# Kernel optimization log

Hardware: AMD Instinct MI355X
Metric: run time of the kernel (lower is better)

## Reference

```python
import jax, jax.numpy as jnp
import numpy as np
import math

B, S, D = 4, 1024, 1024
H, DH = 16, 64
DFF = 4 * D
NEG = -1e9


def _layernorm(x, g, b, eps=1e-5):
    mu = jnp.mean(x, axis=-1, keepdims=True)
    var = jnp.var(x, axis=-1, keepdims=True)
    return (x - mu) * jax.lax.rsqrt(var + eps) * g + b


def setup_inputs() -> dict:
    key = jax.random.key(0)
    ks = jax.random.split(key, 12)
    inp = {
        "input": jax.random.normal(ks[0], (B, S, D), dtype=jnp.float32),
        # additive causal mask: 0 on/below diagonal, -1e9 above
        "causal_mask": jnp.where(
            jnp.tril(jnp.ones((S, S), dtype=bool)), 0.0, NEG
        ).astype(jnp.float32)[None, None],
        # additive padding mask: last 64 tokens of each sequence are padding
        "padding_mask": jnp.where(jnp.arange(S) < S - 64, 0.0, NEG)
        .astype(jnp.float32)[None, None, None, :]
        .repeat(B, axis=0),
        "ln1_g": jnp.ones((D,), jnp.float32), "ln1_b": jnp.zeros((D,), jnp.float32),
        "ln2_g": jnp.ones((D,), jnp.float32), "ln2_b": jnp.zeros((D,), jnp.float32),
        "ln3_g": jnp.ones((D,), jnp.float32), "ln3_b": jnp.zeros((D,), jnp.float32),
        "Wq": jax.random.normal(ks[1], (D, H * DH), jnp.float32) * 0.02,
        "bq": jnp.zeros((H * DH,), jnp.float32),
        "Wk": jax.random.normal(ks[2], (D, H * DH), jnp.float32) * 0.02,
        "bk": jnp.zeros((H * DH,), jnp.float32),
        "Wv": jax.random.normal(ks[3], (D, H * DH), jnp.float32) * 0.02,
        "bv": jnp.zeros((H * DH,), jnp.float32),
        "Wo": jax.random.normal(ks[4], (H * DH, D), jnp.float32) * 0.02,
        "bo": jnp.zeros((D,), jnp.float32),
        "W1": jax.random.normal(ks[5], (D, DFF), jnp.float32) * 0.02,
        "b1": jnp.zeros((DFF,), jnp.float32),
        "W2": jax.random.normal(ks[6], (DFF, D), jnp.float32) * 0.02,
        "b2": jnp.zeros((D,), jnp.float32),
    }
    return inp


def reference(input, causal_mask, padding_mask,
              ln1_g, ln1_b, ln2_g, ln2_b, ln3_g, ln3_b,
              Wq, bq, Wk, bk, Wv, bv, Wo, bo, W1, b1, W2, b2):
    x = _layernorm(input, ln1_g, ln1_b)
    b, s, _ = x.shape

    def heads(y):  # [b,s,H*DH] -> [b,H,s,DH]
        return y.reshape(b, s, H, DH).transpose(0, 2, 1, 3)

    q = heads(x @ Wq + bq)
    k = heads(x @ Wk + bk)
    v = heads(x @ Wv + bv)

    logits = jnp.einsum('bhqd,bhkd->bhqk', q, k) / math.sqrt(DH)
    logits = logits + causal_mask + padding_mask
    probs = jax.nn.softmax(logits, axis=-1)
    attn = jnp.einsum('bhqk,bhkd->bhqd', probs, v)
    attn = attn.transpose(0, 2, 1, 3).reshape(b, s, H * DH)  # b s (h d)
    attn_out = attn @ Wo + bo

    x = x + _layernorm(attn_out, ln2_g, ln2_b)
    h = _layernorm(x, ln3_g, ln3_b)
    x = x + (jax.nn.gelu(h @ W1 + b1, approximate=False) @ W2 + b2)
    return x
```

## Files before the change

kernel.cpp:

```cpp
#include <hip/hip_runtime.h>
#include <hip/hip_bf16.h>

typedef __hip_bfloat16 bf16;
typedef __bf16 bf16x8 __attribute__((ext_vector_type(8)));
typedef float f32x4 __attribute__((ext_vector_type(4)));

#define DEV __device__ __forceinline__

DEV int swz(int r, int k) { return r * 64 + (k ^ ((r & 7) << 3)); }

#define GLOAD_LDS16(gaddr, laddr)                                              \
  __builtin_amdgcn_global_load_lds(                                            \
      (const __attribute__((address_space(1))) void*)(gaddr),                  \
      (__attribute__((address_space(3))) void*)(laddr), 16, 0, 0)

__global__ void prep_kernel(
    const float* __restrict__ Wq, const float* __restrict__ Wk,
    const float* __restrict__ Wv, const float* __restrict__ Wo,
    const float* __restrict__ W1, const float* __restrict__ W2,
    const float* __restrict__ bq, const float* __restrict__ bk,
    const float* __restrict__ bv,
    bf16* __restrict__ WqkvT, bf16* __restrict__ WoT,
    bf16* __restrict__ W1T, bf16* __restrict__ W2T, float* __restrict__ bqkv) {
  int bid = blockIdx.x;
  if (bid >= 12288) {
    int i = (bid - 12288) * 256 + threadIdx.y * 32 + threadIdx.x;
    if (i < 3072)
      bqkv[i] = i < 1024 ? bq[i] : (i < 2048 ? bk[i - 1024] : bv[i - 2048]);
    return;
  }
  const float* src; bf16* dst; int K, N, tb;
  if (bid < 4096) {
    int wsel = bid >> 10;
    src = wsel == 0 ? Wq : wsel == 1 ? Wk : wsel == 2 ? Wv : Wo;
    dst = wsel < 3 ? WqkvT + (size_t)wsel * 1048576 : WoT;
    K = 1024; N = 1024; tb = bid & 1023;
  } else if (bid < 8192) {
    src = W1; dst = W1T; K = 1024; N = 4096; tb = bid - 4096;
  } else {
    src = W2; dst = W2T; K = 4096; N = 1024; tb = bid - 8192;
  }
  int ntx = N >> 5;
  int bx = (tb % ntx) * 32, by = (tb / ntx) * 32;
  __shared__ bf16 t[32][33];
  int tx = threadIdx.x, ty = threadIdx.y;
#pragma unroll
  for (int j = 0; j < 32; j += 8)
    t[ty + j][tx] = __float2bfloat16(src[(size_t)(by + ty + j) * N + bx + tx]);
  __syncthreads();
#pragma unroll
  for (int j = 0; j < 32; j += 8)
    dst[(size_t)(bx + ty + j) * K + by + tx] = t[tx][ty + j];
}

__global__ __launch_bounds__(256) void ln1_kernel(
    const float* __restrict__ in, const float* __restrict__ g, const float* __restrict__ b,
    float* __restrict__ xo, bf16* __restrict__ xb) {
  int row = blockIdx.x, tid = threadIdx.x;
  int lane = tid & 63, w = tid >> 6;
  float4 v = reinterpret_cast<const float4*>(in + (size_t)row * 1024)[tid];
  float s = v.x + v.y + v.z + v.w;
  float sq = v.x * v.x + v.y * v.y + v.z * v.z + v.w * v.w;
#pragma unroll
  for (int m = 32; m; m >>= 1) { s += __shfl_xor(s, m); sq += __shfl_xor(sq, m); }
  __shared__ float ss[4], qq[4];
  if (lane == 0) { ss[w] = s; qq[w] = sq; }
  __syncthreads();
  s = ss[0] + ss[1] + ss[2] + ss[3];
  sq = qq[0] + qq[1] + qq[2] + qq[3];
  float mu = s * (1.f / 1024.f);
  float rs = rsqrtf(sq * (1.f / 1024.f) - mu * mu + 1e-5f);
  float4 gg = reinterpret_cast<const float4*>(g)[tid];
  float4 bb = reinterpret_cast<const float4*>(b)[tid];
  float4 y;
  y.x = (v.x - mu) * rs * gg.x + bb.x;
  y.y = (v.y - mu) * rs * gg.y + bb.y;
  y.z = (v.z - mu) * rs * gg.z + bb.z;
  y.w = (v.w - mu) * rs * gg.w + bb.w;
  reinterpret_cast<float4*>(xo + (size_t)row * 1024)[tid] = y;
  union { bf16 h[4]; uint2 u; } pk;
  pk.h[0] = __float2bfloat16(y.x); pk.h[1] = __float2bfloat16(y.y);
  pk.h[2] = __float2bfloat16(y.z); pk.h[3] = __float2bfloat16(y.w);
  reinterpret_cast<uint2*>(xb + (size_t)row * 1024)[tid] = pk.u;
}

__global__ __launch_bounds__(256) void ln23_kernel(
    const float* __restrict__ x, const float* __restrict__ ao,
    const float* __restrict__ g2, const float* __restrict__ b2,
    const float* __restrict__ g3, const float* __restrict__ b3,
    float* __restrict__ x2o, bf16* __restrict__ hb) {
  int row = blockIdx.x, tid = threadIdx.x;
  int lane = tid & 63, w = tid >> 6;
  float4 a = reinterpret_cast<const float4*>(ao + (size_t)row * 1024)[tid];
  float s = a.x + a.y + a.z + a.w;
  float sq = a.x * a.x + a.y * a.y + a.z * a.z + a.w * a.w;
#pragma unroll
  for (int m = 32; m; m >>= 1) { s += __shfl_xor(s, m); sq += __shfl_xor(sq, m); }
  __shared__ float s1[4], q1[4], s2[4], q2[4];
  if (lane == 0) { s1[w] = s; q1[w] = sq; }
  __syncthreads();
  s = s1[0] + s1[1] + s1[2] + s1[3];
  sq = q1[0] + q1[1] + q1[2] + q1[3];
  float mu = s * (1.f / 1024.f);
  float rs = rsqrtf(sq * (1.f / 1024.f) - mu * mu + 1e-5f);
  float4 xr = reinterpret_cast<const float4*>(x + (size_t)row * 1024)[tid];
  float4 gg = reinterpret_cast<const float4*>(g2)[tid];
  float4 bb = reinterpret_cast<const float4*>(b2)[tid];
  float4 x2;
  x2.x = xr.x + (a.x - mu) * rs * gg.x + bb.x;
  x2.y = xr.y + (a.y - mu) * rs * gg.y + bb.y;
  x2.z = xr.z + (a.z - mu) * rs * gg.z + bb.z;
  x2.w = xr.w + (a.w - mu) * rs * gg.w + bb.w;
  reinterpret_cast<float4*>(x2o + (size_t)row * 1024)[tid] = x2;
  s = x2.x + x2.y + x2.z + x2.w;
  sq = x2.x * x2.x + x2.y * x2.y + x2.z * x2.z + x2.w * x2.w;
#pragma unroll
  for (int m = 32; m; m >>= 1) { s += __shfl_xor(s, m); sq += __shfl_xor(sq, m); }
  if (lane == 0) { s2[w] = s; q2[w] = sq; }
  __syncthreads();
  s = s2[0] + s2[1] + s2[2] + s2[3];
  sq = q2[0] + q2[1] + q2[2] + q2[3];
  mu = s * (1.f / 1024.f);
  rs = rsqrtf(sq * (1.f / 1024.f) - mu * mu + 1e-5f);
  gg = reinterpret_cast<const float4*>(g3)[tid];
  bb = reinterpret_cast<const float4*>(b3)[tid];
  union { bf16 h[4]; uint2 u; } pk;
  pk.h[0] = __float2bfloat16((x2.x - mu) * rs * gg.x + bb.x);
  pk.h[1] = __float2bfloat16((x2.y - mu) * rs * gg.y + bb.y);
  pk.h[2] = __float2bfloat16((x2.z - mu) * rs * gg.z + bb.z);
  pk.h[3] = __float2bfloat16((x2.w - mu) * rs * gg.w + bb.w);
  reinterpret_cast<uint2*>(hb + (size_t)row * 1024)[tid] = pk.u;
}

template <int TS, int WM, int WN, bool GELU, bool RES, bool OUTBF, bool VSPLIT>
__global__ __launch_bounds__(WM * WN * 64, 1) void gemm_8ph(
    const bf16* __restrict__ A, const bf16* __restrict__ BT,
    const float* __restrict__ bias, const float* __restrict__ res,
    float* __restrict__ outf, bf16* __restrict__ outb,
    bf16* __restrict__ kt, bf16* __restrict__ vt,
    int M, int N, int K) {
  constexpr int NW = WM * WN;
  constexpr int RH = TS / WM / 2;
  constexpr int MT2 = RH / 16;
  constexpr int NT = TS / WN / 16;
  __shared__ __align__(16) bf16 LDS[2][4][TS * 32];
  const int t = threadIdx.x, lane = t & 63, w = t >> 6;
  const int wr = w / WN, wc = w % WN;
  const int l15 = lane & 15, l4 = lane >> 4;
  const int gx = gridDim.x, nwg = gx * gridDim.y;
  int bid = blockIdx.y * gx + blockIdx.x;
  int sbid = (bid & 7) * (nwg >> 3) + (bid >> 3);
  const int m0 = (sbid / gx) * TS, n0 = (sbid % gx) * TS;
  const int srow = lane >> 2;
  const int scol8 = (((lane & 3) ^ ((lane >> 3) & 3)) << 3);
  const int ldrd = l15 * 32 + ((l4 ^ ((l15 >> 1) & 3)) << 3);

  auto stage_half = [&](int buf, int tile, int h) {
    const bf16* P = (h & 1) ? BT : A;
    const int rb = (h & 1) ? n0 : m0;
    const int col = (tile << 6) + ((h >> 1) << 5) + scol8;
#pragma unroll
    for (int i = 0; i < 2; ++i) {
      int c = w * 2 + i;
      GLOAD_LDS16(P + (size_t)(rb + c * 16 + srow) * K + col, &LDS[buf][h][c * 512]);
    }
  };

  f32x4 acc[2 * MT2][NT] = {};
  bf16x8 bfr[NT];

  auto phase = [&](int cb, int ks, int mh, int stg_tile, int stg_h, int vm) {
    const bf16* Ah = &LDS[cb][ks * 2][0];
    if (mh == 0) {
      const bf16* Bh = &LDS[cb][ks * 2 + 1][0];
#pragma unroll
      for (int n = 0; n < NT; ++n)
        bfr[n] = *reinterpret_cast<const bf16x8*>(Bh + (wc * (TS / WN) + n * 16) * 32 + ldrd);
    }
    bf16x8 af[MT2];
#pragma unroll
    for (int m = 0; m < MT2; ++m)
      af[m] = *reinterpret_cast<const bf16x8*>(
          Ah + (wr * (TS / WM) + mh * RH + m * 16) * 32 + ldrd);
    if (stg_h >= 0) stage_half(cb ^ 1, stg_tile, stg_h);
    asm volatile("s_barrier" ::: "memory");
    __builtin_amdgcn_sched_barrier(0);
    __builtin_amdgcn_s_setprio(1);
#pragma unroll
    for (int m = 0; m < MT2; ++m)
#pragma unroll
      for (int n = 0; n < NT; ++n)
        acc[mh * MT2 + m][n] =
            __builtin_amdgcn_mfma_f32_16x16x32_bf16(af[m], bfr[n], acc[mh * MT2 + m][n], 0, 0, 0);
    __builtin_amdgcn_s_setprio(0);
    if (vm == 4) asm volatile("s_waitcnt vmcnt(4)" ::: "memory");
    if (vm == 0) asm volatile("s_waitcnt vmcnt(0)" ::: "memory");
    asm volatile("s_barrier" ::: "memory");
  };

  const int nk = K >> 6;
#pragma unroll
  for (int h = 0; h < 4; ++h) stage_half(0, 0, h);
  asm volatile("s_waitcnt vmcnt(4)" ::: "memory");
  asm volatile("s_barrier" ::: "memory");

  for (int tt = 0; tt < nk - 1; ++tt) {
    const int cb = tt & 1;
    phase(cb, 0, 0, tt + 1, 0, -1);
    phase(cb, 0, 1, tt + 1, 1, 4);
    phase(cb, 1, 0, tt + 1, 2, -1);
    phase(cb, 1, 1, tt + 1, 3, 4);
  }
  {
    const int cb = (nk - 1) & 1;
    phase(cb, 0, 0, 0, -1, -1);
    phase(cb, 0, 1, 0, -1, 0);
    phase(cb, 1, 0, 0, -1, -1);
    phase(cb, 1, 1, 0, -1, -1);
  }

#pragma unroll
  for (int mi = 0; mi < 2 * MT2; ++mi) {
    int gr0 = m0 + wr * (TS / WM) + mi * 16 + l4 * 4;
#pragma unroll
    for (int n = 0; n < NT; ++n) {
      int gc = n0 + wc * (TS / WN) + n * 16 + l15;
      float bv = bias[gc];
#pragma unroll
      for (int q = 0; q < 4; ++q) {
        int gr = gr0 + q;
        float v = acc[mi][n][q] + bv;
        if constexpr (GELU) v = 0.5f * v * (1.f + erff(v * 0.70710678118654752f));
        if constexpr (RES) v += res[(size_t)gr * N + gc];
        if constexpr (VSPLIT) {
          int s = gr & 1023, bb = gr >> 10;
          if (gc < 1024) {
            outb[(size_t)gr * N + gc] = __float2bfloat16(v);
          } else if (gc < 2048) {
            int hd = gc - 1024, hh = hd >> 6, d = hd & 63;
            int ln = (s & 15) | (((d >> 3) & 3) << 4);
            kt[(((size_t)(bb * 16 + hh) * 64 + (s >> 4)) << 10) + (d >> 5) * 512 +
               ln * 8 + (d & 7)] = __float2bfloat16(v);
          } else {
            int hd = gc - 2048, hh = hd >> 6, d = hd & 63;
            int ln = (d & 15) | (((s >> 3) & 3) << 4);
            vt[(((size_t)(bb * 16 + hh) * 4 + (d >> 4)) << 14) + ((s >> 5) << 9) +
               ln * 8 + (s & 7)] = __float2bfloat16(v);
          }
        } else if constexpr (OUTBF) {
          outb[(size_t)gr * N + gc] = __float2bfloat16(v);
        } else {
          outf[(size_t)gr * N + gc] = v;
        }
      }
    }
  }
}

template <int BM, int BN, int WM, int WN, int MINW,
          bool GELU, bool RES, bool OUTBF>
__global__ __launch_bounds__(WM * WN * 64, MINW) void gemm_db(
    const bf16* __restrict__ A, const bf16* __restrict__ BT,
    const float* __restrict__ bias, const float* __restrict__ res,
    float* __restrict__ outf, bf16* __restrict__ outb,
    int M, int N, int K) {
  constexpr int NW = WM * WN;
  constexpr int MT = BM / WM / 16, NT = BN / WN / 16;
  constexpr int ACH = BM / 8, BCH = BN / 8;
  constexpr int PW = (ACH + BCH) / NW;
  __shared__ __align__(16) bf16 As[2][BM * 64];
  __shared__ __align__(16) bf16 Bs[2][BN * 64];
  const int t = threadIdx.x, lane = t & 63, w = t >> 6;
  const int wr = w / WN, wc = w % WN;
  const int l15 = lane & 15, l4 = lane >> 4;
  const int gx = gridDim.x, nwg = gx * gridDim.y;
  int bid = blockIdx.y * gx + blockIdx.x;
  int sbid = (bid & 7) * (nwg >> 3) + (bid >> 3);
  const int m0 = (sbid / gx) * BM, n0 = (sbid % gx) * BN;
  const int lr = lane >> 3;
  const int scol = ((lane & 7) * 8) ^ (lr * 8);

  auto stage = [&](int buf, int kt_) {
    const int k0 = kt_ << 6;
#pragma unroll
    for (int i = 0; i < PW; ++i) {
      int c = w * PW + i;
      if (c < ACH) {
        GLOAD_LDS16(A + (size_t)(m0 + c * 8 + lr) * K + k0 + scol, &As[buf][c * 512]);
      } else {
        int c2 = c - ACH;
        GLOAD_LDS16(BT + (size_t)(n0 + c2 * 8 + lr) * K + k0 + scol, &Bs[buf][c2 * 512]);
      }
    }
  };

  f32x4 acc[MT][NT] = {};
  const int nk = K >> 6;
  stage(0, 0);
  __syncthreads();
  int cur = 0;
  for (int kk = 0; kk < nk; ++kk) {
    if (kk + 1 < nk) stage(cur ^ 1, kk + 1);
#pragma unroll
    for (int ks = 0; ks < 2; ++ks) {
      bf16x8 af[MT], bfr[NT];
#pragma unroll
      for (int m = 0; m < MT; ++m)
        af[m] = *reinterpret_cast<const bf16x8*>(
            &As[cur][swz(wr * (BM / WM) + m * 16 + l15, ks * 32 + l4 * 8)]);
#pragma unroll
      for (int n = 0; n < NT; ++n)
        bfr[n] = *reinterpret_cast<const bf16x8*>(
            &Bs[cur][swz(wc * (BN / WN) + n * 16 + l15, ks * 32 + l4 * 8)]);
      __builtin_amdgcn_s_setprio(1);
#pragma unroll
      for (int m = 0; m < MT; ++m)
#pragma unroll
        for (int n = 0; n < NT; ++n)
          acc[m][n] = __builtin_amdgcn_mfma_f32_16x16x32_bf16(af[m], bfr[n], acc[m][n], 0, 0, 0);
      __builtin_amdgcn_s_setprio(0);
    }
    __syncthreads();
    cur ^= 1;
  }

#pragma unroll
  for (int m = 0; m < MT; ++m) {
    int gr0 = m0 + wr * (BM / WM) + m * 16 + l4 * 4;
#pragma unroll
    for (int n = 0; n < NT; ++n) {
      int gc = n0 + wc * (BN / WN) + n * 16 + l15;
      float bv = bias[gc];
#pragma unroll
      for (int q = 0; q < 4; ++q) {
        int gr = gr0 + q;
        float v = acc[m][n][q] + bv;
        if constexpr (GELU) v = 0.5f * v * (1.f + erff(v * 0.70710678118654752f));
        if constexpr (RES) v += res[(size_t)gr * N + gc];
        if constexpr (OUTBF) outb[(size_t)gr * N + gc] = __float2bfloat16(v);
        else                 outf[(size_t)gr * N + gc] = v;
      }
    }
  }
}

__global__ __launch_bounds__(256, 2) void attn_kernel(
    const bf16* __restrict__ qkv, const bf16* __restrict__ kt,
    const bf16* __restrict__ vt, bf16* __restrict__ o) {
  const int S = 1024, QS = 3072, HD = 1024;
  const bf16* qg = qkv;
  int bid = blockIdx.x;
  int xcd = bid & 7, j = bid >> 3;
  int grp = xcd * 8 + (j >> 3);
  int pr = j & 7;
  const int b = grp >> 4, h = grp & 15;
  const int t = threadIdx.x, lane = t & 63, w = t >> 6;
  const int l15 = lane & 15, l4 = lane >> 4;

  constexpr int PSTR = 72;
  __shared__ __align__(16) bf16 P[4][16 * PSTR];

  const int bh = b * 16 + h;
  const bf16* kbase = kt + ((size_t)bh << 16) + lane * 8;
  const bf16* vbase = vt + ((size_t)bh << 16) + lane * 8;

  bf16x8 kA[8], kB[8];
  auto loadK = [&](int kb, bf16x8* kf) {
#pragma unroll
    for (int cb = 0; cb < 4; ++cb)
#pragma unroll
      for (int ks = 0; ks < 2; ++ks)
        kf[cb * 2 + ks] = *reinterpret_cast<const bf16x8*>(
            kbase + (((kb >> 4) + cb) << 10) + (ks << 9));
  };

  auto run_strip = [&](int q0) {
    bf16x8 qf0, qf1;
    {
      const bf16* qp = qg + (size_t)(b * S + q0 + l15) * QS + h * 64 + l4 * 8;
      qf0 = *reinterpret_cast<const bf16x8*>(qp);
      qf1 = *reinterpret_cast<const bf16x8*>(qp + 32);
    }
    f32x4 acc[4] = {};
    float mrow = -1e30f, lrow = 0.f;
    const int kmaxa = q0 + 15, kmax = kmaxa < 959 ? kmaxa : 959;
    const int nt = (kmax >> 6) + 1;
    loadK(0, kA);

    for (int kt_ = 0; kt_ < nt; ++kt_) {
      const int kb = kt_ << 6;
      bf16x8* kf = (kt_ & 1) ? kB : kA;
      bf16x8* kn = (kt_ & 1) ? kA : kB;
      bf16x8 vf[8];
#pragma unroll
      for (int n = 0; n < 4; ++n)
#pragma unroll
        for (int ks = 0; ks < 2; ++ks)
          vf[n * 2 + ks] = *reinterpret_cast<const bf16x8*>(
              vbase + (n << 14) + (((kb >> 5) + ks) << 9));
      if (kt_ + 1 < nt) loadK(kb + 64, kn);

      f32x4 sc[4];
      __builtin_amdgcn_s_setprio(1);
#pragma unroll
      for (int cb = 0; cb < 4; ++cb) {
        f32x4 z = {};
        z = __builtin_amdgcn_mfma_f32_16x16x32_bf16(kf[cb * 2 + 0], qf0, z, 0, 0, 0);
        z = __builtin_amdgcn_mfma_f32_16x16x32_bf16(kf[cb * 2 + 1], qf1, z, 0, 0, 0);
        sc[cb] = z;
      }
      __builtin_amdgcn_s_setprio(0);

      const int q = q0 + l15;
      float p[16];
#pragma unroll
      for (int cb = 0; cb < 4; ++cb)
#pragma unroll
        for (int r = 0; r < 4; ++r) {
          int kgl = kb + cb * 16 + l4 * 4 + r;
          p[cb * 4 + r] = (kgl > q) ? -1e30f : sc[cb][r] * 0.125f;
        }
      float tm = p[0];
#pragma unroll
      for (int i = 1; i < 16; ++i) tm = fmaxf(tm, p[i]);
      tm = fmaxf(tm, __shfl_xor(tm, 16));
      tm = fmaxf(tm, __shfl_xor(tm, 32));
      bool defer = __all(tm <= mrow + 8.f);
      float mn = defer ? mrow : fmaxf(mrow, tm);
      float ps = 0.f;
#pragma unroll
      for (int i = 0; i < 16; ++i) { p[i] = __expf(p[i] - mn); ps += p[i]; }
      ps += __shfl_xor(ps, 16);
      ps += __shfl_xor(ps, 32);
      if (defer) {
        lrow += ps;
      } else {
        float al = __expf(mrow - mn);
        mrow = mn;
        lrow = lrow * al + ps;
#pragma unroll
        for (int n = 0; n < 4; ++n)
#pragma unroll
          for (int r = 0; r < 4; ++r) acc[n][r] *= al;
      }
#pragma unroll
      for (int cb = 0; cb < 4; ++cb) {
        union { bf16 h4[4]; uint2 u; } pk;
#pragma unroll
        for (int r = 0; r < 4; ++r) pk.h4[r] = __float2bfloat16(p[cb * 4 + r]);
        *reinterpret_cast<uint2*>(&P[w][l15 * PSTR + cb * 16 + l4 * 4]) = pk.u;
      }
      asm volatile("" ::: "memory");
      bf16x8 pb0 = *reinterpret_cast<const bf16x8*>(&P[w][l15 * PSTR + l4 * 8]);
      bf16x8 pb1 = *reinterpret_cast<const bf16x8*>(&P[w][l15 * PSTR + 32 + l4 * 8]);
      __builtin_amdgcn_s_setprio(1);
#pragma unroll
      for (int n = 0; n < 4; ++n) {
        acc[n] = __builtin_amdgcn_mfma_f32_16x16x32_bf16(vf[n * 2 + 0], pb0, acc[n], 0, 0, 0);
        acc[n] = __builtin_amdgcn_mfma_f32_16x16x32_bf16(vf[n * 2 + 1], pb1, acc[n], 0, 0, 0);
      }
      __builtin_amdgcn_s_setprio(0);
    }

    float inv = 1.f / lrow;
#pragma unroll
    for (int n = 0; n < 4; ++n) {
      union { bf16 h4[4]; uint2 u; } pk;
#pragma unroll
      for (int r = 0; r < 4; ++r) pk.h4[r] = __float2bfloat16(acc[n][r] * inv);
      *reinterpret_cast<uint2*>(&P[w][l15 * PSTR + n * 16 + l4 * 4]) = pk.u;
    }
    asm volatile("" ::: "memory");
    {
      int qq = lane >> 2, c = lane & 3;
#pragma unroll
      for (int i = 0; i < 2; ++i) {
        uint4 ov = *reinterpret_cast<const uint4*>(&P[w][qq * PSTR + c * 16 + i * 8]);
        *reinterpret_cast<uint4*>(
            o + (size_t)(b * S + q0 + qq) * HD + h * 64 + c * 16 + i * 8) = ov;
      }
    }
    asm volatile("" ::: "memory");
  };

  run_strip(pr * 64 + w * 16);
  run_strip((15 - pr) * 64 + w * 16);
}

extern "C" void kernel_launch(void* const* d_in, const int* in_sizes, int n_in,
                              void* d_out, int out_size, void* d_ws, size_t ws_size,
                              hipStream_t stream) {
  const float* input = (const float*)d_in[0];
  const float* ln1g = (const float*)d_in[3];
  const float* ln1b = (const float*)d_in[4];
  const float* ln2g = (const float*)d_in[5];
  const float* ln2b = (const float*)d_in[6];
  const float* ln3g = (const float*)d_in[7];
  const float* ln3b = (const float*)d_in[8];
  const float* Wq = (const float*)d_in[9];  const float* bq = (const float*)d_in[10];
  const float* Wk = (const float*)d_in[11]; const float* bk = (const float*)d_in[12];
  const float* Wv = (const float*)d_in[13]; const float* bv = (const float*)d_in[14];
  const float* Wo = (const float*)d_in[15]; const float* bo = (const float*)d_in[16];
  const float* W1 = (const float*)d_in[17]; const float* b1 = (const float*)d_in[18];
  const float* W2 = (const float*)d_in[19]; const float* b2 = (const float*)d_in[20];

  const int M = 4096, D = 1024, F = 4096;
  char* p = (char*)d_ws;
  size_t off = 0;
  auto nxt = [&](size_t n) { char* r = p + off; off += n; return r; };
  bf16* WqkvT = (bf16*)nxt((size_t)3 * D * D * 2);
  bf16* WoT = (bf16*)nxt((size_t)D * D * 2);
  bf16* W1T = (bf16*)nxt((size_t)F * D * 2);
  bf16* W2T = (bf16*)nxt((size_t)D * F * 2);
  float* bqkv = (float*)nxt(16384);
  float* xf  = (float*)nxt((size_t)M * D * 4);
  float* aof = (float*)nxt((size_t)M * D * 4);
  float* x2f = (float*)nxt((size_t)M * D * 4);
  bf16* xb = (bf16*)nxt((size_t)M * D * 2);
  bf16* qkv = (bf16*)nxt((size_t)M * 3 * D * 2);
  bf16* ktb = (bf16*)aof;
  bf16* vtb = (bf16*)((char*)aof + (size_t)8 * 1024 * 1024);
  bf16* gb = (bf16*)xf;
  bf16* ab = xb;
  bf16* hb = qkv;

  prep_kernel<<<12300, dim3(32, 8), 0, stream>>>(
      Wq, Wk, Wv, Wo, W1, W2, bq, bk, bv, WqkvT, WoT, W1T, W2T, bqkv);

  ln1_kernel<<<M, 256, 0, stream>>>(input, ln1g, ln1b, xf, xb);

  gemm_8ph<256, 2, 4, false, false, true, true><<<dim3(12, 16), 512, 0, stream>>>(
      xb, WqkvT, bqkv, nullptr, nullptr, qkv, ktb, vtb, M, 3 * D, D);

  attn_kernel<<<512, 256, 0, stream>>>(qkv, ktb, vtb, ab);

  gemm_db<128, 64, 2, 2, 4, false, false, false>
      <<<dim3(16, 32), 256, 0, stream>>>(
      ab, WoT, bo, nullptr, aof, nullptr, M, D, D);

  ln23_kernel<<<M, 256, 0, stream>>>(xf, aof, ln2g, ln2b, ln3g, ln3b, x2f, hb);

  gemm_8ph<256, 2, 4, true, false, true, false><<<dim3(16, 16), 512, 0, stream>>>(
      hb, W1T, b1, nullptr, nullptr, gb, nullptr, nullptr, M, F, D);
  gemm_8ph<128, 2, 2, false, true, false, false><<<dim3(8, 32), 256, 0, stream>>>(
      gb, W2T, b2, x2f, (float*)d_out, nullptr, nullptr, nullptr, M, D, F);
}
```

Baseline: 221.4 us.

## Fold LN1 into prep kernel and move QKV GEMM to 256x192 double-buffered kernel

Merges the LN1 row normalization into the weight-prep launch as extra blocks, which removes one kernel launch. The QKV projection moves from the 8-phase 256x256 GEMM to the simpler double-buffered gemm_db with 256x192 tiles, so the 16x16 grid covers 256 workgroups instead of 192, and the VSPLIT K/V transpose epilogue moves with it. The sched_barrier in the 8-phase GEMM phase loop is also removed, giving the compiler freedom to reorder around the MFMA block. The trade-off is that the QKV GEMM gives up the finer-grained 8-phase pipelining.

```diff
diff --git a/kernel.cpp b/kernel.cpp
--- a/kernel.cpp
+++ b/kernel.cpp
@@ -21,8 +21,40 @@
     const float* __restrict__ bq, const float* __restrict__ bk,
     const float* __restrict__ bv,
     bf16* __restrict__ WqkvT, bf16* __restrict__ WoT,
-    bf16* __restrict__ W1T, bf16* __restrict__ W2T, float* __restrict__ bqkv) {
+    bf16* __restrict__ W1T, bf16* __restrict__ W2T, float* __restrict__ bqkv,
+    const float* __restrict__ in, const float* __restrict__ g1,
+    const float* __restrict__ b1v, float* __restrict__ xo, bf16* __restrict__ xb) {
+  __shared__ bf16 t[32][33];
+  __shared__ float ss[4], qq[4];
   int bid = blockIdx.x;
+  if (bid >= 12300) {
+    int row = bid - 12300, tid = threadIdx.y * 32 + threadIdx.x;
+    int lane = tid & 63, w = tid >> 6;
+    float4 v = reinterpret_cast<const float4*>(in + (size_t)row * 1024)[tid];
+    float s = v.x + v.y + v.z + v.w;
+    float sq = v.x * v.x + v.y * v.y + v.z * v.z + v.w * v.w;
+#pragma unroll
+    for (int m = 32; m; m >>= 1) { s += __shfl_xor(s, m); sq += __shfl_xor(sq, m); }
+    if (lane == 0) { ss[w] = s; qq[w] = sq; }
+    __syncthreads();
+    s = ss[0] + ss[1] + ss[2] + ss[3];
+    sq = qq[0] + qq[1] + qq[2] + qq[3];
+    float mu = s * (1.f / 1024.f);
+    float rs = rsqrtf(sq * (1.f / 1024.f) - mu * mu + 1e-5f);
+    float4 gg = reinterpret_cast<const float4*>(g1)[tid];
+    float4 bb = reinterpret_cast<const float4*>(b1v)[tid];
+    float4 y;
+    y.x = (v.x - mu) * rs * gg.x + bb.x;
+    y.y = (v.y - mu) * rs * gg.y + bb.y;
+    y.z = (v.z - mu) * rs * gg.z + bb.z;
+    y.w = (v.w - mu) * rs * gg.w + bb.w;
+    reinterpret_cast<float4*>(xo + (size_t)row * 1024)[tid] = y;
+    union { bf16 h[4]; uint2 u; } pk;
+    pk.h[0] = __float2bfloat16(y.x); pk.h[1] = __float2bfloat16(y.y);
+    pk.h[2] = __float2bfloat16(y.z); pk.h[3] = __float2bfloat16(y.w);
+    reinterpret_cast<uint2*>(xb + (size_t)row * 1024)[tid] = pk.u;
+    return;
+  }
   if (bid >= 12288) {
     int i = (bid - 12288) * 256 + threadIdx.y * 32 + threadIdx.x;
     if (i < 3072)
@@ -42,7 +74,6 @@
   }
   int ntx = N >> 5;
   int bx = (tb % ntx) * 32, by = (tb / ntx) * 32;
-  __shared__ bf16 t[32][33];
   int tx = threadIdx.x, ty = threadIdx.y;
 #pragma unroll
   for (int j = 0; j < 32; j += 8)
@@ -51,37 +82,6 @@
 #pragma unroll
   for (int j = 0; j < 32; j += 8)
     dst[(size_t)(bx + ty + j) * K + by + tx] = t[tx][ty + j];
-}
-
-__global__ __launch_bounds__(256) void ln1_kernel(
-    const float* __restrict__ in, const float* __restrict__ g, const float* __restrict__ b,
-    float* __restrict__ xo, bf16* __restrict__ xb) {
-  int row = blockIdx.x, tid = threadIdx.x;
-  int lane = tid & 63, w = tid >> 6;
-  float4 v = reinterpret_cast<const float4*>(in + (size_t)row * 1024)[tid];
-  float s = v.x + v.y + v.z + v.w;
-  float sq = v.x * v.x + v.y * v.y + v.z * v.z + v.w * v.w;
-#pragma unroll
-  for (int m = 32; m; m >>= 1) { s += __shfl_xor(s, m); sq += __shfl_xor(sq, m); }
-  __shared__ float ss[4], qq[4];
-  if (lane == 0) { ss[w] = s; qq[w] = sq; }
-  __syncthreads();
-  s = ss[0] + ss[1] + ss[2] + ss[3];
-  sq = qq[0] + qq[1] + qq[2] + qq[3];
-  float mu = s * (1.f / 1024.f);
-  float rs = rsqrtf(sq * (1.f / 1024.f) - mu * mu + 1e-5f);
-  float4 gg = reinterpret_cast<const float4*>(g)[tid];
-  float4 bb = reinterpret_cast<const float4*>(b)[tid];
-  float4 y;
-  y.x = (v.x - mu) * rs * gg.x + bb.x;
-  y.y = (v.y - mu) * rs * gg.y + bb.y;
-  y.z = (v.z - mu) * rs * gg.z + bb.z;
-  y.w = (v.w - mu) * rs * gg.w + bb.w;
-  reinterpret_cast<float4*>(xo + (size_t)row * 1024)[tid] = y;
-  union { bf16 h[4]; uint2 u; } pk;
-  pk.h[0] = __float2bfloat16(y.x); pk.h[1] = __float2bfloat16(y.y);
-  pk.h[2] = __float2bfloat16(y.z); pk.h[3] = __float2bfloat16(y.w);
-  reinterpret_cast<uint2*>(xb + (size_t)row * 1024)[tid] = pk.u;
 }
 
 __global__ __launch_bounds__(256) void ln23_kernel(
@@ -132,14 +132,12 @@
   reinterpret_cast<uint2*>(hb + (size_t)row * 1024)[tid] = pk.u;
 }
 
-template <int TS, int WM, int WN, bool GELU, bool RES, bool OUTBF, bool VSPLIT>
+template <int TS, int WM, int WN, bool GELU, bool RES, bool OUTBF>
 __global__ __launch_bounds__(WM * WN * 64, 1) void gemm_8ph(
     const bf16* __restrict__ A, const bf16* __restrict__ BT,
     const float* __restrict__ bias, const float* __restrict__ res,
     float* __restrict__ outf, bf16* __restrict__ outb,
-    bf16* __restrict__ kt, bf16* __restrict__ vt,
     int M, int N, int K) {
-  constexpr int NW = WM * WN;
   constexpr int RH = TS / WM / 2;
   constexpr int MT2 = RH / 16;
   constexpr int NT = TS / WN / 16;
@@ -184,7 +182,6 @@
           Ah + (wr * (TS / WM) + mh * RH + m * 16) * 32 + ldrd);
     if (stg_h >= 0) stage_half(cb ^ 1, stg_tile, stg_h);
     asm volatile("s_barrier" ::: "memory");
-    __builtin_amdgcn_sched_barrier(0);
     __builtin_amdgcn_s_setprio(1);
 #pragma unroll
     for (int m = 0; m < MT2; ++m)
@@ -230,6 +227,94 @@
       for (int q = 0; q < 4; ++q) {
         int gr = gr0 + q;
         float v = acc[mi][n][q] + bv;
+        if constexpr (GELU) v = 0.5f * v * (1.f + erff(v * 0.70710678118654752f));
+        if constexpr (RES) v += res[(size_t)gr * N + gc];
+        if constexpr (OUTBF) outb[(size_t)gr * N + gc] = __float2bfloat16(v);
+        else                 outf[(size_t)gr * N + gc] = v;
+      }
+    }
+  }
+}
+
+template <int BM, int BN, int WM, int WN, int MINW,
+          bool GELU, bool RES, bool OUTBF, bool VSPLIT>
+__global__ __launch_bounds__(WM * WN * 64, MINW) void gemm_db(
+    const bf16* __restrict__ A, const bf16* __restrict__ BT,
+    const float* __restrict__ bias, const float* __restrict__ res,
+    float* __restrict__ outf, bf16* __restrict__ outb,
+    bf16* __restrict__ kt, bf16* __restrict__ vt,
+    int M, int N, int K) {
+  constexpr int NW = WM * WN;
+  constexpr int MT = BM / WM / 16, NT = BN / WN / 16;
+  constexpr int ACH = BM / 8, BCH = BN / 8;
+  constexpr int PW = (ACH + BCH) / NW;
+  __shared__ __align__(16) bf16 As[2][BM * 64];
+  __shared__ __align__(16) bf16 Bs[2][BN * 64];
+  const int t = threadIdx.x, lane = t & 63, w = t >> 6;
+  const int wr = w / WN, wc = w % WN;
+  const int l15 = lane & 15, l4 = lane >> 4;
+  const int gx = gridDim.x, nwg = gx * gridDim.y;
+  int bid = blockIdx.y * gx + blockIdx.x;
+  int sbid = (bid & 7) * (nwg >> 3) + (bid >> 3);
+  const int m0 = (sbid / gx) * BM, n0 = (sbid % gx) * BN;
+  const int lr = lane >> 3;
+  const int scol = ((lane & 7) * 8) ^ (lr * 8);
+
+  auto stage = [&](int buf, int kt_) {
+    const int k0 = kt_ << 6;
+#pragma unroll
+    for (int i = 0; i < PW; ++i) {
+      int c = w * PW + i;
+      if (c < ACH) {
+        GLOAD_LDS16(A + (size_t)(m0 + c * 8 + lr) * K + k0 + scol, &As[buf][c * 512]);
+      } else {
+        int c2 = c - ACH;
+        GLOAD_LDS16(BT + (size_t)(n0 + c2 * 8 + lr) * K + k0 + scol, &Bs[buf][c2 * 512]);
+      }
+    }
+  };
+
+  f32x4 acc[MT][NT] = {};
+  const int nk = K >> 6;
+  stage(0, 0);
+  __syncthreads();
+  int cur = 0;
+  for (int kk = 0; kk < nk; ++kk) {
+    if (kk + 1 < nk) stage(cur ^ 1, kk + 1);
+#pragma unroll
+    for (int ks = 0; ks < 2; ++ks) {
+      bf16x8 af[MT], bfr[NT];
+#pragma unroll
+      for (int m = 0; m < MT; ++m)
+        af[m] = *reinterpret_cast<const bf16x8*>(
+            &As[cur][swz(wr * (BM / WM) + m * 16 + l15, ks * 32 + l4 * 8)]);
+#pragma unroll
+      for (int n = 0; n < NT; ++n)
+        bfr[n] = *reinterpret_cast<const bf16x8*>(
+            &Bs[cur][swz(wc * (BN / WN) + n * 16 + l15, ks * 32 + l4 * 8)]);
+      __builtin_amdgcn_s_setprio(1);
+#pragma unroll
+      for (int m = 0; m < MT; ++m)
+#pragma unroll
+        for (int n = 0; n < NT; ++n)
+          acc[m][n] = __builtin_amdgcn_mfma_f32_16x16x32_bf16(af[m], bfr[n], acc[m][n], 0, 0, 0);
+      __builtin_amdgcn_s_setprio(0);
+    }
+    __syncthreads();
+    cur ^= 1;
+  }
+
+#pragma unroll
+  for (int m = 0; m < MT; ++m) {
+    int gr0 = m0 + wr * (BM / WM) + m * 16 + l4 * 4;
+#pragma unroll
+    for (int n = 0; n < NT; ++n) {
+      int gc = n0 + wc * (BN / WN) + n * 16 + l15;
+      float bv = bias[gc];
+#pragma unroll
+      for (int q = 0; q < 4; ++q) {
+        int gr = gr0 + q;
+        float v = acc[m][n][q] + bv;
         if constexpr (GELU) v = 0.5f * v * (1.f + erff(v * 0.70710678118654752f));
         if constexpr (RES) v += res[(size_t)gr * N + gc];
         if constexpr (VSPLIT) {
@@ -257,93 +342,6 @@
   }
 }
 
-template <int BM, int BN, int WM, int WN, int MINW,
-          bool GELU, bool RES, bool OUTBF>
-__global__ __launch_bounds__(WM * WN * 64, MINW) void gemm_db(
-    const bf16* __restrict__ A, const bf16* __restrict__ BT,
-    const float* __restrict__ bias, const float* __restrict__ res,
-    float* __restrict__ outf, bf16* __restrict__ outb,
-    int M, int N, int K) {
-  constexpr int NW = WM * WN;
-  constexpr int MT = BM / WM / 16, NT = BN / WN / 16;
-  constexpr int ACH = BM / 8, BCH = BN / 8;
-  constexpr int PW = (ACH + BCH) / NW;
-  __shared__ __align__(16) bf16 As[2][BM * 64];
-  __shared__ __align__(16) bf16 Bs[2][BN * 64];
-  const int t = threadIdx.x, lane = t & 63, w = t >> 6;
-  const int wr = w / WN, wc = w % WN;
-  const int l15 = lane & 15, l4 = lane >> 4;
-  const int gx = gridDim.x, nwg = gx * gridDim.y;
-  int bid = blockIdx.y * gx + blockIdx.x;
-  int sbid = (bid & 7) * (nwg >> 3) + (bid >> 3);
-  const int m0 = (sbid / gx) * BM, n0 = (sbid % gx) * BN;
-  const int lr = lane >> 3;
-  const int scol = ((lane & 7) * 8) ^ (lr * 8);
-
-  auto stage = [&](int buf, int kt_) {
-    const int k0 = kt_ << 6;
-#pragma unroll
-    for (int i = 0; i < PW; ++i) {
-      int c = w * PW + i;
-      if (c < ACH) {
-        GLOAD_LDS16(A + (size_t)(m0 + c * 8 + lr) * K + k0 + scol, &As[buf][c * 512]);
-      } else {
-        int c2 = c - ACH;
-        GLOAD_LDS16(BT + (size_t)(n0 + c2 * 8 + lr) * K + k0 + scol, &Bs[buf][c2 * 512]);
-      }
-    }
-  };
-
-  f32x4 acc[MT][NT] = {};
-  const int nk = K >> 6;
-  stage(0, 0);
-  __syncthreads();
-  int cur = 0;
-  for (int kk = 0; kk < nk; ++kk) {
-    if (kk + 1 < nk) stage(cur ^ 1, kk + 1);
-#pragma unroll
-    for (int ks = 0; ks < 2; ++ks) {
-      bf16x8 af[MT], bfr[NT];
-#pragma unroll
-      for (int m = 0; m < MT; ++m)
-        af[m] = *reinterpret_cast<const bf16x8*>(
-            &As[cur][swz(wr * (BM / WM) + m * 16 + l15, ks * 32 + l4 * 8)]);
-#pragma unroll
-      for (int n = 0; n < NT; ++n)
-        bfr[n] = *reinterpret_cast<const bf16x8*>(
-            &Bs[cur][swz(wc * (BN / WN) + n * 16 + l15, ks * 32 + l4 * 8)]);
-      __builtin_amdgcn_s_setprio(1);
-#pragma unroll
-      for (int m = 0; m < MT; ++m)
-#pragma unroll
-        for (int n = 0; n < NT; ++n)
-          acc[m][n] = __builtin_amdgcn_mfma_f32_16x16x32_bf16(af[m], bfr[n], acc[m][n], 0, 0, 0);
-      __builtin_amdgcn_s_setprio(0);
-    }
-    __syncthreads();
-    cur ^= 1;
-  }
-
-#pragma unroll
-  for (int m = 0; m < MT; ++m) {
-    int gr0 = m0 + wr * (BM / WM) + m * 16 + l4 * 4;
-#pragma unroll
-    for (int n = 0; n < NT; ++n) {
-      int gc = n0 + wc * (BN / WN) + n * 16 + l15;
-      float bv = bias[gc];
-#pragma unroll
-      for (int q = 0; q < 4; ++q) {
-        int gr = gr0 + q;
-        float v = acc[m][n][q] + bv;
-        if constexpr (GELU) v = 0.5f * v * (1.f + erff(v * 0.70710678118654752f));
-        if constexpr (RES) v += res[(size_t)gr * N + gc];
-        if constexpr (OUTBF) outb[(size_t)gr * N + gc] = __float2bfloat16(v);
-        else                 outf[(size_t)gr * N + gc] = v;
-      }
-    }
-  }
-}
-
 __global__ __launch_bounds__(256, 2) void attn_kernel(
     const bf16* __restrict__ qkv, const bf16* __restrict__ kt,
     const bf16* __restrict__ vt, bf16* __restrict__ o) {
@@ -524,24 +522,24 @@
   bf16* ab = xb;
   bf16* hb = qkv;
 
-  prep_kernel<<<12300, dim3(32, 8), 0, stream>>>(
-      Wq, Wk, Wv, Wo, W1, W2, bq, bk, bv, WqkvT, WoT, W1T, W2T, bqkv);
-
-  ln1_kernel<<<M, 256, 0, stream>>>(input, ln1g, ln1b, xf, xb);
-
-  gemm_8ph<256, 2, 4, false, false, true, true><<<dim3(12, 16), 512, 0, stream>>>(
+  prep_kernel<<<12300 + 4096, dim3(32, 8), 0, stream>>>(
+      Wq, Wk, Wv, Wo, W1, W2, bq, bk, bv, WqkvT, WoT, W1T, W2T, bqkv,
+      input, ln1g, ln1b, xf, xb);
+
+  gemm_db<256, 192, 2, 4, 1, false, false, true, true>
+      <<<dim3(16, 16), 512, 0, stream>>>(
       xb, WqkvT, bqkv, nullptr, nullptr, qkv, ktb, vtb, M, 3 * D, D);
 
   attn_kernel<<<512, 256, 0, stream>>>(qkv, ktb, vtb, ab);
 
-  gemm_db<128, 64, 2, 2, 4, false, false, false>
+  gemm_db<128, 64, 2, 2, 4, false, false, false, false>
       <<<dim3(16, 32), 256, 0, stream>>>(
-      ab, WoT, bo, nullptr, aof, nullptr, M, D, D);
+      ab, WoT, bo, nullptr, aof, nullptr, nullptr, nullptr, M, D, D);
 
   ln23_kernel<<<M, 256, 0, stream>>>(xf, aof, ln2g, ln2b, ln3g, ln3b, x2f, hb);
 
-  gemm_8ph<256, 2, 4, true, false, true, false><<<dim3(16, 16), 512, 0, stream>>>(
-      hb, W1T, b1, nullptr, nullptr, gb, nullptr, nullptr, M, F, D);
-  gemm_8ph<128, 2, 2, false, true, false, false><<<dim3(8, 32), 256, 0, stream>>>(
-      gb, W2T, b2, x2f, (float*)d_out, nullptr, nullptr, nullptr, M, D, F);
+  gemm_8ph<256, 2, 4, true, false, true><<<dim3(16, 16), 512, 0, stream>>>(
+      hb, W1T, b1, nullptr, nullptr, gb, M, F, D);
+  gemm_8ph<128, 2, 2, false, true, false><<<dim3(8, 32), 256, 0, stream>>>(
+      gb, W2T, b2, x2f, (float*)d_out, nullptr, M, D, F);
 }
```

After: 214.1 us. -3.3%, faster.
